# Kernel optimization log

Measured on AMD Instinct MI355X. Metric: run time of the kernel, lower is better.

Reference implementation:

```python
import jax, jax.numpy as jnp
import numpy as np

B = 1024      # batch of ego samples (one query each)
N = 32768     # flat pool of neighbor hidden states
H = 256       # hidden_dim == feat_dim
MAX_NEIGH = 64


def setup_inputs() -> dict:
    key = jax.random.key(0)
    ks = jax.random.split(key, 10)
    enc_hidden = jax.random.normal(ks[0], (B, H), dtype=jnp.float32)
    social_ht = jax.random.normal(ks[1], (N, H), dtype=jnp.float32)
    starts = jax.random.randint(ks[2], (B,), 0, N - MAX_NEIGH)
    lens = jax.random.randint(ks[3], (B,), 1, MAX_NEIGH)  # >=1 neighbor per sample
    ends = starts + lens
    w_scale = 1.0 / np.sqrt(H)
    Wq = jax.random.normal(ks[4], (H, H), dtype=jnp.float32) * w_scale
    Wk = jax.random.normal(ks[5], (H, H), dtype=jnp.float32) * w_scale
    Wv = jax.random.normal(ks[6], (H, H), dtype=jnp.float32) * w_scale
    bq = jax.random.normal(ks[7], (H,), dtype=jnp.float32) * w_scale
    bk = jax.random.normal(ks[8], (H,), dtype=jnp.float32) * w_scale
    bv = jax.random.normal(ks[9], (H,), dtype=jnp.float32) * w_scale
    return {
        "enc_hidden": enc_hidden, "social_ht": social_ht,
        "neighbors_idx_start": starts, "neighbors_idx_end": ends,
        "Wq": Wq, "bq": bq, "Wk": Wk, "bk": bk, "Wv": Wv, "bv": bv,
    }


def reference(enc_hidden, social_ht, neighbors_idx_start, neighbors_idx_end,
              Wq, bq, Wk, bk, Wv, bv):
    d = Wq.shape[1]
    inv_sqrt_d = 1.0 / jnp.sqrt(jnp.asarray(d, enc_hidden.dtype))
    # q_emb / k_emb / v_emb are Linear + ReLU; q is scaled AFTER the ReLU
    q = jax.nn.relu(enc_hidden @ Wq + bq) * inv_sqrt_d      # [B, H]
    k = jax.nn.relu(social_ht @ Wk + bk)                     # [N, H]
    v = jax.nn.relu(social_ht @ Wv + bv)                     # [N, H]
    scores = q @ k.T                                         # [B, N]
    pos = jnp.arange(social_ht.shape[0])                     # [N]
    # mask: sample i attends only to social_ht[start_i:end_i]
    mask = (pos[None, :] >= neighbors_idx_start[:, None]) & \
           (pos[None, :] < neighbors_idx_end[:, None])       # [B, N]
    attn = jax.nn.softmax(jnp.where(mask, scores, -jnp.inf), axis=-1)
    return attn @ v                                          # [B, H]
```

## Files before the change

### kernel.cpp

```cpp
#include <hip/hip_runtime.h>
#include <hip/hip_bf16.h>
#include <math.h>

#define H 256
#define BQ 1024
#define NPOOL 32768
#define MAXN 64

typedef __attribute__((ext_vector_type(8))) short short8;
typedef __attribute__((ext_vector_type(8))) unsigned short ushort8v;
typedef __attribute__((ext_vector_type(4))) float f32x4;

__device__ __forceinline__ unsigned short f2bf(float f) {
  unsigned int u = __float_as_uint(f);
  unsigned int r = (u + 0x7fffu + ((u >> 16) & 1u)) >> 16;
  return (unsigned short)r;
}
__device__ __forceinline__ float b2f(unsigned short u) {
  return __uint_as_float((unsigned int)u << 16);
}
__device__ __forceinline__ unsigned int cvt_pk_bf16(float a, float b) {
  unsigned int r;
  asm("v_cvt_pk_bf16_f32 %0, %1, %2" : "=v"(r) : "v"(a), "v"(b));
  return r;
}
__device__ __forceinline__ void gload16(const void* g, void* l) {
  __builtin_amdgcn_global_load_lds(
      (const __attribute__((address_space(1))) unsigned int*)g,
      (__attribute__((address_space(3))) unsigned int*)l, 16, 0, 0);
}

__global__ __launch_bounds__(256) void prep_kernel(
    const float* __restrict__ Wq, const float* __restrict__ Wk,
    const float* __restrict__ Wv, const float* __restrict__ bq,
    unsigned short* __restrict__ WqT, unsigned short* __restrict__ WkT,
    unsigned short* __restrict__ WvT, float* __restrict__ bqs) {
  __shared__ float ls[64][65];
  const int b = blockIdx.x;
  const int t = threadIdx.x;
  const float* W = (b < 16) ? Wq : ((b < 32) ? Wk : Wv);
  unsigned short* WT = (b < 16) ? WqT : ((b < 32) ? WkT : WvT);
  const float scale = (b < 16) ? 0.0625f : 1.0f;
  const int tile = b & 15;
  const int k0 = (tile >> 2) * 64, c0 = (tile & 3) * 64;
  const int tx = t & 63, ty = t >> 6;
#pragma unroll
  for (int kk = 0; kk < 16; ++kk)
    ls[tx][kk * 4 + ty] = W[(size_t)(k0 + kk * 4 + ty) * H + c0 + tx];
  __syncthreads();
#pragma unroll
  for (int cc = 0; cc < 16; ++cc) {
    const int c = cc * 4 + ty;
    WT[(size_t)(c0 + c) * H + k0 + tx] = f2bf(ls[c][tx] * scale);
  }
  if (b < 4 && t < 64) bqs[c0 + t] = bq[c0 + t] * 0.0625f;
}

__global__ __launch_bounds__(512) void gemm_kernel(
    const float* __restrict__ soc, const float* __restrict__ enc,
    const unsigned short* __restrict__ WkT,
    const unsigned short* __restrict__ WvT,
    const unsigned short* __restrict__ WqT,
    const float* __restrict__ bk, const float* __restrict__ bv,
    const float* __restrict__ bqs,
    unsigned short* __restrict__ kout, unsigned short* __restrict__ vout,
    unsigned short* __restrict__ qout) {
  __shared__ __align__(16) char LDSb[98304];
  const int t = threadIdx.x;
  const int lane = t & 63, wid = t >> 6;
  const int bid = blockIdx.x;
  const bool isQ = bid >= 512;
  int brow, col0;
  if (isQ) {
    const int tl = bid - 512;
    brow = (tl >> 1) * 128;
    col0 = (tl & 1) * 128;
  } else {
    const int bx = ((bid >> 4) << 3) | (bid & 7);
    const int by = (bid >> 3) & 1;
    brow = bx * 128;
    col0 = by * 128;
  }
  const float* Asrc = isQ ? enc : soc;
  const unsigned short* Bkg = isQ ? WqT : WkT;
  const unsigned short* Bvg = isQ ? WqT : WvT;
  const float* biask = isQ ? bqs : bk;
  const float* biasv = isQ ? bqs : bv;
  unsigned short* outk = isQ ? qout : kout;
  unsigned short* outv = isQ ? qout : vout;

  const int srow = t >> 3;
  const int slin = t & 7;
  const int arow = t >> 2;
  const int sbase = (t & 3) * 2;

  f32x4 accK[2][4], accV[2][4];
#pragma unroll
  for (int n = 0; n < 2; ++n)
#pragma unroll
    for (int m = 0; m < 4; ++m) { accK[n][m] = (f32x4)0.f; accV[n][m] = (f32x4)0.f; }

  const int wr = wid >> 2, wc = wid & 3;

  float4 av[4];
  const float* asrc = Asrc + (size_t)(brow + arow) * H + sbase * 8;

#define AREG_LOAD(kt)                                                 \
  {                                                                   \
    const float* p_ = asrc + (kt)*64;                                 \
    _Pragma("unroll") for (int s = 0; s < 4; ++s)                     \
        av[s] = *(const float4*)(p_ + s * 4);                         \
  }
#define STAGE_B(kt, pb)                                               \
  {                                                                   \
    const int k0_ = (kt)*64;                                          \
    char* bk_ = LDSb + 32768 + (pb)*16384;                            \
    char* bv_ = LDSb + 65536 + (pb)*16384;                            \
    _Pragma("unroll") for (int c = 0; c < 2; ++c) {                   \
      const int row_ = c * 64 + srow;                                 \
      const int ssrc_ = slin ^ (row_ & 7);                            \
      gload16(Bkg + (size_t)(col0 + row_) * H + k0_ + ssrc_ * 8,      \
              bk_ + c * 8192 + t * 16);                               \
      gload16(Bvg + (size_t)(col0 + row_) * H + k0_ + ssrc_ * 8,      \
              bv_ + c * 8192 + t * 16);                               \
    }                                                                 \
  }
#define AWRITE(pb)                                                    \
  {                                                                   \
    char* ab_ = LDSb + (pb)*16384;                                    \
    _Pragma("unroll") for (int s = 0; s < 2; ++s) {                   \
      uint4 p;                                                        \
      p.x = cvt_pk_bf16(av[2 * s].x, av[2 * s].y);                    \
      p.y = cvt_pk_bf16(av[2 * s].z, av[2 * s].w);                    \
      p.z = cvt_pk_bf16(av[2 * s + 1].x, av[2 * s + 1].y);            \
      p.w = cvt_pk_bf16(av[2 * s + 1].z, av[2 * s + 1].w);            \
      *(uint4*)(ab_ + arow * 128 + ((sbase + s) ^ (arow & 7)) * 16) = p; \
    }                                                                 \
  }

  AREG_LOAD(0);
  STAGE_B(0, 0);
  asm volatile("s_waitcnt vmcnt(4)" ::: "memory");
  AWRITE(0);

#pragma unroll
  for (int kt = 0; kt < 4; ++kt) {
    const int cur = kt & 1;
    if (kt < 3) {
      AREG_LOAD(kt + 1);
      STAGE_B(kt + 1, cur ^ 1);
      asm volatile("s_waitcnt vmcnt(8)" ::: "memory");
    } else {
      asm volatile("s_waitcnt vmcnt(0)" ::: "memory");
    }
    asm volatile("s_waitcnt lgkmcnt(0)" ::: "memory");
    __builtin_amdgcn_s_barrier();
    const char* Ab = LDSb + cur * 16384;
    const char* Bkb = LDSb + 32768 + cur * 16384;
    const char* Bvb = LDSb + 65536 + cur * 16384;
#pragma unroll
    for (int kk = 0; kk < 2; ++kk) {
      short8 af[4], bkf[2], bvf[2];
#pragma unroll
      for (int m = 0; m < 4; ++m) {
        const int ar = wr * 64 + m * 16 + (lane & 15);
        const int sl = (kk * 4 + (lane >> 4)) ^ (ar & 7);
        af[m] = *(const short8*)(Ab + ar * 128 + sl * 16);
      }
#pragma unroll
      for (int n = 0; n < 2; ++n) {
        const int br = wc * 32 + n * 16 + (lane & 15);
        const int sl = (kk * 4 + (lane >> 4)) ^ (br & 7);
        bkf[n] = *(const short8*)(Bkb + br * 128 + sl * 16);
        bvf[n] = *(const short8*)(Bvb + br * 128 + sl * 16);
      }
#pragma unroll
      for (int n = 0; n < 2; ++n)
#pragma unroll
        for (int m = 0; m < 4; ++m) {
          accK[n][m] = __builtin_amdgcn_mfma_f32_16x16x32_bf16(
              af[m], bkf[n], accK[n][m], 0, 0, 0);
          accV[n][m] = __builtin_amdgcn_mfma_f32_16x16x32_bf16(
              af[m], bvf[n], accV[n][m], 0, 0, 0);
        }
    }
    if (kt < 3) {
      asm volatile("s_waitcnt vmcnt(4)" ::: "memory");
      AWRITE(cur ^ 1);
    }
    __builtin_amdgcn_s_barrier();
  }
#undef AREG_LOAD
#undef STAGE_B
#undef AWRITE

  float bkn[2], bvn[2];
#pragma unroll
  for (int n = 0; n < 2; ++n) {
    const int col = col0 + wc * 32 + n * 16 + (lane & 15);
    bkn[n] = biask[col]; bvn[n] = biasv[col];
  }
#pragma unroll
  for (int n = 0; n < 2; ++n)
#pragma unroll
    for (int m = 0; m < 4; ++m) {
      const int col = col0 + wc * 32 + n * 16 + (lane & 15);
#pragma unroll
      for (int r = 0; r < 4; ++r) {
        const int row = brow + wr * 64 + m * 16 + (lane >> 4) * 4 + r;
        outk[(size_t)row * H + col] = f2bf(fmaxf(accK[n][m][r] + bkn[n], 0.f));
        outv[(size_t)row * H + col] = f2bf(fmaxf(accV[n][m][r] + bvn[n], 0.f));
      }
    }
}

__global__ __launch_bounds__(256) void attn_kernel(
    const unsigned short* __restrict__ qb,
    const unsigned short* __restrict__ kb,
    const unsigned short* __restrict__ vb, const int* __restrict__ starts,
    const int* __restrict__ ends, float* __restrict__ out) {
  __shared__ float sc[MAXN];
  const int row = blockIdx.x, t = threadIdx.x;
  const int lane = t & 63, wave = t >> 6;
  const int start = starts[row];
  const int len = ends[row] - start;

  const int qp = (lane & 31) * 8;
  const ushort8v q8 = *(const ushort8v*)(qb + (size_t)row * H + qp);
  float qf[8];
#pragma unroll
  for (int e = 0; e < 8; ++e) qf[e] = b2f(q8[e]);

  for (int jj = wave * 2; jj < len; jj += 8) {
    const int j0 = jj + (lane >> 5);
    if (j0 < len) {
      const ushort8v k8 =
          *(const ushort8v*)(kb + (size_t)(start + j0) * H + qp);
      float s = qf[0] * b2f(k8[0]) + qf[1] * b2f(k8[1]) +
                qf[2] * b2f(k8[2]) + qf[3] * b2f(k8[3]) +
                qf[4] * b2f(k8[4]) + qf[5] * b2f(k8[5]) +
                qf[6] * b2f(k8[6]) + qf[7] * b2f(k8[7]);
#pragma unroll
      for (int off = 16; off; off >>= 1) s += __shfl_xor(s, off, 64);
      if ((lane & 31) == 0) sc[j0] = s;
    }
  }
  __syncthreads();

  if (t < 64) {
    const float x = (t < len) ? sc[t] : -INFINITY;
    float m = x;
#pragma unroll
    for (int off = 32; off; off >>= 1) m = fmaxf(m, __shfl_xor(m, off, 64));
    const float p = (t < len) ? __expf(x - m) : 0.f;
    float ssum = p;
#pragma unroll
    for (int off = 32; off; off >>= 1) ssum += __shfl_xor(ssum, off, 64);
    sc[t] = p / ssum;
  }
  __syncthreads();

  const unsigned short* vp = vb + (size_t)start * H + t;
  float a0 = 0.f, a1 = 0.f, a2 = 0.f, a3 = 0.f;
  int j = 0;
  for (; j + 3 < len; j += 4) {
    a0 = fmaf(sc[j + 0], b2f(vp[(size_t)(j + 0) * H]), a0);
    a1 = fmaf(sc[j + 1], b2f(vp[(size_t)(j + 1) * H]), a1);
    a2 = fmaf(sc[j + 2], b2f(vp[(size_t)(j + 2) * H]), a2);
    a3 = fmaf(sc[j + 3], b2f(vp[(size_t)(j + 3) * H]), a3);
  }
  for (; j < len; ++j) a0 = fmaf(sc[j], b2f(vp[(size_t)j * H]), a0);
  out[(size_t)row * H + t] = (a0 + a1) + (a2 + a3);
}

extern "C" void kernel_launch(void* const* d_in, const int* in_sizes, int n_in,
                              void* d_out, int out_size, void* d_ws,
                              size_t ws_size, hipStream_t stream) {
  (void)in_sizes; (void)n_in; (void)out_size; (void)ws_size;
  const float* enc = (const float*)d_in[0];
  const float* soc = (const float*)d_in[1];
  const int* starts = (const int*)d_in[2];
  const int* ends = (const int*)d_in[3];
  const float* Wq = (const float*)d_in[4];
  const float* bq = (const float*)d_in[5];
  const float* Wk = (const float*)d_in[6];
  const float* bk = (const float*)d_in[7];
  const float* Wv = (const float*)d_in[8];
  const float* bv = (const float*)d_in[9];
  float* out = (float*)d_out;

  unsigned short* kb = (unsigned short*)d_ws;
  unsigned short* vb = kb + (size_t)NPOOL * H;
  unsigned short* WkT = vb + (size_t)NPOOL * H;
  unsigned short* WvT = WkT + H * H;
  unsigned short* WqT = WvT + H * H;
  unsigned short* qbf = WqT + H * H;
  float* bqs = (float*)(qbf + (size_t)BQ * H);

  prep_kernel<<<48, 256, 0, stream>>>(Wq, Wk, Wv, bq, WqT, WkT, WvT, bqs);
  gemm_kernel<<<528, 512, 0, stream>>>(soc, enc, WkT, WvT, WqT, bk, bv, bqs,
                                       kb, vb, qbf);
  attn_kernel<<<BQ, 256, 0, stream>>>(qbf, kb, vb, starts, ends, out);
}
```

Measured before the change: 49.00 us.

## Retile projection GEMM to 64-row blocks covering all 256 output columns

The K/V/Q projection GEMM tile changes from 128 rows by 128 columns to 64 rows by the full 256 columns. Each block now reads its fp32 activation rows once instead of twice, and the bf16 conversion of A is no longer duplicated across column blocks. The cost is twice as much weight traffic staged per block and an LDS footprint of 144KB per block, which limits occupancy to one block per CU. Launch grid and wait counts are adjusted to match.

Measured after the change: 49.14 us. About the same (+0.3%).

```diff
diff --git a/kernel.cpp b/kernel.cpp
--- a/kernel.cpp
+++ b/kernel.cpp
@@ -65,22 +65,12 @@
     const float* __restrict__ bqs,
     unsigned short* __restrict__ kout, unsigned short* __restrict__ vout,
     unsigned short* __restrict__ qout) {
-  __shared__ __align__(16) char LDSb[98304];
+  __shared__ __align__(16) char LDSb[147456];
   const int t = threadIdx.x;
   const int lane = t & 63, wid = t >> 6;
   const int bid = blockIdx.x;
   const bool isQ = bid >= 512;
-  int brow, col0;
-  if (isQ) {
-    const int tl = bid - 512;
-    brow = (tl >> 1) * 128;
-    col0 = (tl & 1) * 128;
-  } else {
-    const int bx = ((bid >> 4) << 3) | (bid & 7);
-    const int by = (bid >> 3) & 1;
-    brow = bx * 128;
-    col0 = by * 128;
-  }
+  const int brow = (isQ ? (bid - 512) : bid) * 64;
   const float* Asrc = isQ ? enc : soc;
   const unsigned short* Bkg = isQ ? WqT : WkT;
   const unsigned short* Bvg = isQ ? WqT : WvT;
@@ -89,58 +79,54 @@
   unsigned short* outk = isQ ? qout : kout;
   unsigned short* outv = isQ ? qout : vout;
 
-  const int srow = t >> 3;
-  const int slin = t & 7;
-  const int arow = t >> 2;
-  const int sbase = (t & 3) * 2;
-
-  f32x4 accK[2][4], accV[2][4];
-#pragma unroll
-  for (int n = 0; n < 2; ++n)
-#pragma unroll
-    for (int m = 0; m < 4; ++m) { accK[n][m] = (f32x4)0.f; accV[n][m] = (f32x4)0.f; }
+  const int arow = t >> 3;
+  const int aslot = t & 7;
+
+  f32x4 accK[4][2], accV[4][2];
+#pragma unroll
+  for (int n = 0; n < 4; ++n)
+#pragma unroll
+    for (int m = 0; m < 2; ++m) { accK[n][m] = (f32x4)0.f; accV[n][m] = (f32x4)0.f; }
 
   const int wr = wid >> 2, wc = wid & 3;
 
-  float4 av[4];
-  const float* asrc = Asrc + (size_t)(brow + arow) * H + sbase * 8;
+  float4 av[2];
+  const float* asrc = Asrc + (size_t)(brow + arow) * H + aslot * 8;
 
 #define AREG_LOAD(kt)                                                 \
   {                                                                   \
     const float* p_ = asrc + (kt)*64;                                 \
-    _Pragma("unroll") for (int s = 0; s < 4; ++s)                     \
-        av[s] = *(const float4*)(p_ + s * 4);                         \
+    av[0] = *(const float4*)(p_);                                     \
+    av[1] = *(const float4*)(p_ + 4);                                 \
   }
 #define STAGE_B(kt, pb)                                               \
   {                                                                   \
     const int k0_ = (kt)*64;                                          \
-    char* bk_ = LDSb + 32768 + (pb)*16384;                            \
-    char* bv_ = LDSb + 65536 + (pb)*16384;                            \
-    _Pragma("unroll") for (int c = 0; c < 2; ++c) {                   \
-      const int row_ = c * 64 + srow;                                 \
-      const int ssrc_ = slin ^ (row_ & 7);                            \
-      gload16(Bkg + (size_t)(col0 + row_) * H + k0_ + ssrc_ * 8,      \
+    char* bk_ = LDSb + 16384 + (pb)*32768;                            \
+    char* bv_ = LDSb + 81920 + (pb)*32768;                            \
+    _Pragma("unroll") for (int c = 0; c < 4; ++c) {                   \
+      const int row_ = c * 64 + arow;                                 \
+      const int ssrc_ = aslot ^ (row_ & 7);                           \
+      gload16(Bkg + (size_t)row_ * H + k0_ + ssrc_ * 8,               \
               bk_ + c * 8192 + t * 16);                               \
-      gload16(Bvg + (size_t)(col0 + row_) * H + k0_ + ssrc_ * 8,      \
+      gload16(Bvg + (size_t)row_ * H + k0_ + ssrc_ * 8,               \
               bv_ + c * 8192 + t * 16);                               \
     }                                                                 \
   }
 #define AWRITE(pb)                                                    \
   {                                                                   \
-    char* ab_ = LDSb + (pb)*16384;                                    \
-    _Pragma("unroll") for (int s = 0; s < 2; ++s) {                   \
-      uint4 p;                                                        \
-      p.x = cvt_pk_bf16(av[2 * s].x, av[2 * s].y);                    \
-      p.y = cvt_pk_bf16(av[2 * s].z, av[2 * s].w);                    \
-      p.z = cvt_pk_bf16(av[2 * s + 1].x, av[2 * s + 1].y);            \
-      p.w = cvt_pk_bf16(av[2 * s + 1].z, av[2 * s + 1].w);            \
-      *(uint4*)(ab_ + arow * 128 + ((sbase + s) ^ (arow & 7)) * 16) = p; \
-    }                                                                 \
+    uint4 p;                                                          \
+    p.x = cvt_pk_bf16(av[0].x, av[0].y);                              \
+    p.y = cvt_pk_bf16(av[0].z, av[0].w);                              \
+    p.z = cvt_pk_bf16(av[1].x, av[1].y);                              \
+    p.w = cvt_pk_bf16(av[1].z, av[1].w);                              \
+    *(uint4*)(LDSb + (pb)*8192 + arow * 128 +                         \
+              (aslot ^ (arow & 7)) * 16) = p;                         \
   }
 
   AREG_LOAD(0);
   STAGE_B(0, 0);
-  asm volatile("s_waitcnt vmcnt(4)" ::: "memory");
+  asm volatile("s_waitcnt vmcnt(8)" ::: "memory");
   AWRITE(0);
 
 #pragma unroll
@@ -149,35 +135,35 @@
     if (kt < 3) {
       AREG_LOAD(kt + 1);
       STAGE_B(kt + 1, cur ^ 1);
-      asm volatile("s_waitcnt vmcnt(8)" ::: "memory");
+      asm volatile("s_waitcnt vmcnt(10)" ::: "memory");
     } else {
       asm volatile("s_waitcnt vmcnt(0)" ::: "memory");
     }
     asm volatile("s_waitcnt lgkmcnt(0)" ::: "memory");
     __builtin_amdgcn_s_barrier();
-    const char* Ab = LDSb + cur * 16384;
-    const char* Bkb = LDSb + 32768 + cur * 16384;
-    const char* Bvb = LDSb + 65536 + cur * 16384;
+    const char* Ab = LDSb + cur * 8192;
+    const char* Bkb = LDSb + 16384 + cur * 32768;
+    const char* Bvb = LDSb + 81920 + cur * 32768;
 #pragma unroll
     for (int kk = 0; kk < 2; ++kk) {
-      short8 af[4], bkf[2], bvf[2];
-#pragma unroll
-      for (int m = 0; m < 4; ++m) {
-        const int ar = wr * 64 + m * 16 + (lane & 15);
+      short8 af[2], bkf[4], bvf[4];
+#pragma unroll
+      for (int m = 0; m < 2; ++m) {
+        const int ar = wr * 32 + m * 16 + (lane & 15);
         const int sl = (kk * 4 + (lane >> 4)) ^ (ar & 7);
         af[m] = *(const short8*)(Ab + ar * 128 + sl * 16);
       }
 #pragma unroll
-      for (int n = 0; n < 2; ++n) {
-        const int br = wc * 32 + n * 16 + (lane & 15);
+      for (int n = 0; n < 4; ++n) {
+        const int br = wc * 64 + n * 16 + (lane & 15);
         const int sl = (kk * 4 + (lane >> 4)) ^ (br & 7);
         bkf[n] = *(const short8*)(Bkb + br * 128 + sl * 16);
         bvf[n] = *(const short8*)(Bvb + br * 128 + sl * 16);
       }
 #pragma unroll
-      for (int n = 0; n < 2; ++n)
-#pragma unroll
-        for (int m = 0; m < 4; ++m) {
+      for (int n = 0; n < 4; ++n)
+#pragma unroll
+        for (int m = 0; m < 2; ++m) {
           accK[n][m] = __builtin_amdgcn_mfma_f32_16x16x32_bf16(
               af[m], bkf[n], accK[n][m], 0, 0, 0);
           accV[n][m] = __builtin_amdgcn_mfma_f32_16x16x32_bf16(
@@ -185,7 +171,7 @@
         }
     }
     if (kt < 3) {
-      asm volatile("s_waitcnt vmcnt(4)" ::: "memory");
+      asm volatile("s_waitcnt vmcnt(8)" ::: "memory");
       AWRITE(cur ^ 1);
     }
     __builtin_amdgcn_s_barrier();
@@ -194,20 +180,20 @@
 #undef STAGE_B
 #undef AWRITE
 
-  float bkn[2], bvn[2];
-#pragma unroll
-  for (int n = 0; n < 2; ++n) {
-    const int col = col0 + wc * 32 + n * 16 + (lane & 15);
+  float bkn[4], bvn[4];
+#pragma unroll
+  for (int n = 0; n < 4; ++n) {
+    const int col = wc * 64 + n * 16 + (lane & 15);
     bkn[n] = biask[col]; bvn[n] = biasv[col];
   }
 #pragma unroll
-  for (int n = 0; n < 2; ++n)
-#pragma unroll
-    for (int m = 0; m < 4; ++m) {
-      const int col = col0 + wc * 32 + n * 16 + (lane & 15);
+  for (int n = 0; n < 4; ++n)
+#pragma unroll
+    for (int m = 0; m < 2; ++m) {
+      const int col = wc * 64 + n * 16 + (lane & 15);
 #pragma unroll
       for (int r = 0; r < 4; ++r) {
-        const int row = brow + wr * 64 + m * 16 + (lane >> 4) * 4 + r;
+        const int row = brow + wr * 32 + m * 16 + (lane >> 4) * 4 + r;
         outk[(size_t)row * H + col] = f2bf(fmaxf(accK[n][m][r] + bkn[n], 0.f));
         outv[(size_t)row * H + col] = f2bf(fmaxf(accV[n][m][r] + bvn[n], 0.f));
       }
```
